# Kernel optimization log

Hardware: AMD Instinct MI355X
Metric: run time of the kernel (lower is better)

## Reference

```python
import jax, jax.numpy as jnp
import numpy as np

E, B, N, F, F1D, H, L, H2, PE_DIM = 4, 16384, 1024, 64, 64, 256, 2, 256, 63
TOPK_MEM = 16      # self.top_K: memory retrieval top-k
W0_SIREN = 30.0    # SIREN omega_0 for 'sine' nonlinearity
NUM_FREQ = 10      # PosEncoding num_frequencies
LINE_DIM = 64      # feat_shapes[0]


def _ln(h, g, b):
    m = jnp.mean(h, axis=-1, keepdims=True)
    v = jnp.mean((h - m) ** 2, axis=-1, keepdims=True)
    return (h - m) / jnp.sqrt(v + 1e-5) * g + b


def _pos_enc(coords):
    # NeRF positional encoding: [coords, sin/cos interleaved per coord per freq]
    freqs = 2.0 ** jnp.arange(NUM_FREQ, dtype=coords.dtype)
    scaled = coords[..., None] * freqs * jnp.pi            # (B, 3, NF)
    sc = jnp.stack([jnp.sin(scaled), jnp.cos(scaled)], axis=-1)  # (B, 3, NF, 2)
    return jnp.concatenate([coords, sc.reshape(coords.shape[0], -1)], axis=-1)  # (B, 63)


def _forward(x, lines, mem_k, mem_v, enc_w0, enc_b0, enc_wh, enc_bh, enc_wo, enc_bo,
             ln_g, ln_b, wq, wk, wv, ad_w0, ad_b0, ad_w1, ad_b1, ad_ln_g, ad_ln_b,
             mg_w0, mg_b0, mg_w1, mg_b1, fw0, fb0, fw1, fb1, fw2, fb2, fw3, fb3, route_k):
    coords = x[:, :3]
    # --- 1D line feature interpolation (param_feats) ---
    p = x[:, 3] * (LINE_DIM - 1)
    pf = jnp.floor(p)
    w = p - pf
    il = pf.astype(jnp.int32)
    ih = jnp.clip(pf + 1.0, 0.0, LINE_DIM - 1).astype(jnp.int32)
    f1d = lines[0][:, il] + w * (lines[0][:, ih] - lines[0][:, il])  # (F1D, B)
    param_feats = f1d.T                                              # (B, F1D)

    pe_x = _pos_enc(coords)                                          # (B, 63)
    scale = float(F) ** 0.5

    def expert(ew0, eb0, ewh, ebh, ewo, ebo, wq_e, wk_e, wv_e, mk, mv,
               aw0, ab0, aw1, ab1, ag, ab):
        # SIREN encoder MLP
        h = jnp.sin(W0_SIREN * (pe_x @ ew0 + eb0))
        for l in range(L):
            h = jnp.sin(W0_SIREN * (h @ ewh[l] + ebh[l]))
        mlp_feats = h @ ewo + ebo                          # (B, F)
        q = _ln(mlp_feats, ln_g, ln_b) @ wq_e              # (B, F)
        kp = mk @ wk_e                                     # (N, F) precomputed keys
        vp = mv @ wv_e                                     # (N, F) precomputed values
        scores = q @ kp.T                                  # (B, N)
        _, idx = jax.lax.top_k(scores, TOPK_MEM)           # (B, K)
        k_top = kp[idx]                                    # (B, K, F)
        v_top = vp[idx]                                    # (B, K, F)
        pfe = jnp.broadcast_to(param_feats[:, None, :], (param_feats.shape[0], TOPK_MEM, F1D))
        a = jnp.concatenate([v_top, pfe], axis=-1)         # (B, K, F+F1D)
        a = jax.nn.relu(a @ aw0 + ab0) @ aw1 + ab1
        adapted = v_top + _ln(a, ag, ab)
        attn = jax.nn.softmax(jnp.einsum('bf,bkf->bk', q, k_top) / scale, axis=-1)
        return jnp.einsum('bk,bkf->bf', attn, adapted) + mlp_feats

    # compute every expert densely (vectorized), then gather routed top-k outputs
    all_out = jax.vmap(expert)(enc_w0, enc_b0, enc_wh, enc_bh, enc_wo, enc_bo,
                               wq, wk, wv, mem_k, mem_v,
                               ad_w0, ad_b0, ad_w1, ad_b1, ad_ln_g, ad_ln_b)  # (E, B, F)

    raw_q = jax.nn.relu(coords @ mg_w0 + mg_b0) @ mg_w1 + mg_b1   # manager_net (B, E)
    probs = jnp.clip(jax.nn.softmax(raw_q, axis=-1), 1e-8, None)
    vals, tidx = jax.lax.top_k(probs, route_k)                    # (B, k)
    vals = vals / jnp.sum(vals, axis=-1, keepdims=True)
    gathered = jnp.take_along_axis(jnp.swapaxes(all_out, 0, 1), tidx[..., None], axis=1)  # (B, k, F)
    spatial = jnp.sum(vals[..., None] * gathered, axis=1)         # (B, F)

    h = jax.nn.relu(spatial @ fw0 + fb0)
    h = jax.nn.relu(h @ fw1 + fb1)
    h = jax.nn.relu(h @ fw2 + fb2)
    refined = jax.nn.sigmoid(h @ fw3 + fb3)
    return refined, raw_q


def setup_inputs() -> dict:
    ks = jax.random.split(jax.random.key(0), 24)
    f32 = jnp.float32
    rn = lambda i, shp, s: jax.random.normal(ks[i], shp, f32) * s
    xav = lambda fi, fo: (2.0 / (fi + fo)) ** 0.5
    return {
        'x': jax.random.uniform(ks[0], (B, 4), f32),
        'lines': jax.random.uniform(ks[1], (1, F1D, LINE_DIM), f32, 0.7, 0.8),
        'mem_k': rn(2, (E, N, F), 1.0),
        'mem_v': rn(3, (E, N, F), 1e-3),
        'enc_w0': rn(4, (E, PE_DIM, H), xav(PE_DIM, H)),
        'enc_b0': jnp.zeros((E, H), f32),
        'enc_wh': rn(5, (E, L, H, H), xav(H, H)),
        'enc_bh': jnp.zeros((E, L, H), f32),
        'enc_wo': rn(6, (E, H, F), xav(H, F)),
        'enc_bo': jnp.zeros((E, F), f32),
        'ln_g': jnp.ones((F,), f32),
        'ln_b': jnp.zeros((F,), f32),
        'wq': rn(7, (E, F, F), xav(F, F)),
        'wk': rn(8, (E, F, F), xav(F, F)),
        'wv': rn(9, (E, F, F), xav(F, F)),
        'ad_w0': rn(10, (E, F + F1D, 64), xav(F + F1D, 64)),
        'ad_b0': rn(11, (E, 64), 1e-3),
        'ad_w1': rn(12, (E, 64, F), xav(64, F)),
        'ad_b1': rn(13, (E, F), 1e-3),
        'ad_ln_g': jnp.ones((E, F), f32),
        'ad_ln_b': jnp.zeros((E, F), f32),
        'mg_w0': rn(14, (3, 64), 0.5),
        'mg_b0': jnp.zeros((64,), f32),
        'mg_w1': rn(15, (64, E), 0.5),
        'mg_b1': jnp.zeros((E,), f32),
        'fw0': rn(16, (F, H2), xav(F, H2)),
        'fb0': rn(17, (H2,), 1e-3),
        'fw1': rn(18, (H2, H2), xav(H2, H2)),
        'fb1': rn(19, (H2,), 1e-3),
        'fw2': rn(20, (H2, H2), xav(H2, H2)),
        'fb2': rn(21, (H2,), 1e-3),
        'fw3': rn(22, (H2, 1), xav(H2, 1)),
        'fb3': rn(23, (1,), 1e-3),
        'route_k': 2,
    }


def reference(x, lines, mem_k, mem_v, enc_w0, enc_b0, enc_wh, enc_bh, enc_wo, enc_bo,
              ln_g, ln_b, wq, wk, wv, ad_w0, ad_b0, ad_w1, ad_b1, ad_ln_g, ad_ln_b,
              mg_w0, mg_b0, mg_w1, mg_b1, fw0, fb0, fw1, fb1, fw2, fb2, fw3, fb3, route_k):
    return _forward(x, lines, mem_k, mem_v, enc_w0, enc_b0, enc_wh, enc_bh, enc_wo, enc_bo,
                    ln_g, ln_b, wq, wk, wv, ad_w0, ad_b0, ad_w1, ad_b1, ad_ln_g, ad_ln_b,
                    mg_w0, mg_b0, mg_w1, mg_b1, fw0, fb0, fw1, fb1, fw2, fb2, fw3, fb3, route_k)
```

## Files before the change

### kernel.cpp

```cpp
#include <hip/hip_runtime.h>
#include <math.h>

#define EE 4
#define BB 16384
#define NN 1024
#define FF 64
#define HH 256
#define PED 63
#define TOPK 16
#define LINE 64
#define TS 32
#define NBX (BB/TS)

#define OFF_KP   0u
#define OFF_VP   262144u
#define OFF_VPA  524288u
#define OFF_PE   786432u
#define OFF_PF   1818624u
#define OFF_EO   2867200u
#define OFF_RW   4964352u
#define OFF_CNT  4997120u
#define OFF_LIST 4997128u
#define OFF_QV   5062664u
#define OFF_SM   7159816u
#define OFF_WP   OFF_EO

__device__ __forceinline__ float wred_sum(float v) {
#pragma unroll
    for (int off = 32; off > 0; off >>= 1) v += __shfl_xor(v, off, 64);
    return v;
}
__device__ __forceinline__ void wred_sum2(float& a, float& b) {
#pragma unroll
    for (int off = 32; off > 0; off >>= 1) {
        a += __shfl_xor(a, off, 64);
        b += __shfl_xor(b, off, 64);
    }
}
__device__ __forceinline__ float rdlane(float v, int k) {
    return __int_as_float(__builtin_amdgcn_readlane(__float_as_int(v), k));
}

__global__ __launch_bounds__(256) void k_prep(
    const float* __restrict__ wv, const float* __restrict__ aw0,
    float* __restrict__ wp)
{
    int e = blockIdx.x;
    __shared__ float sa[FF*FF];
    for (int i = threadIdx.x; i < FF*FF; i += 256)
        sa[i] = aw0[(size_t)e*128*FF + i];
    __syncthreads();
    int f = threadIdx.x & 63, dg = threadIdx.x >> 6;
    for (int d = dg; d < FF; d += 4) {
        const float* wr = wv + (size_t)e*FF*FF + d*FF;
        float a = 0.f;
        for (int c = 0; c < FF; ++c) a = fmaf(wr[c], sa[c*FF+f], a);
        wp[(size_t)e*FF*FF + d*FF + f] = a;
    }
}

__global__ __launch_bounds__(256) void k_proj(
    const float* __restrict__ mem_k, const float* __restrict__ mem_v,
    const float* __restrict__ wk, const float* __restrict__ wv,
    const float* __restrict__ wp,
    float* __restrict__ kp, float* __restrict__ vp, float* __restrict__ vpa)
{
    int e = blockIdx.x >> 6;
    int nbase = (blockIdx.x & 63) * 16;
    __shared__ float swk[FF*FF], swv[FF*FF], swp[FF*FF];
    for (int i = threadIdx.x; i < FF*FF; i += 256) {
        swk[i] = wk[(size_t)e*FF*FF + i];
        swv[i] = wv[(size_t)e*FF*FF + i];
        swp[i] = wp[(size_t)e*FF*FF + i];
    }
    __syncthreads();
    int r4 = threadIdx.x >> 6;
    int f  = threadIdx.x & 63;
#pragma unroll 1
    for (int it = 0; it < 4; ++it) {
        int n = nbase + it*4 + r4;
        const float* mk = mem_k + ((size_t)e*NN + n)*FF;
        const float* mv = mem_v + ((size_t)e*NN + n)*FF;
        float ak = 0.f, av = 0.f, aa = 0.f;
#pragma unroll 1
        for (int c4 = 0; c4 < 16; ++c4) {
            float4 k4 = *(const float4*)&mk[4*c4];
            float4 v4 = *(const float4*)&mv[4*c4];
#pragma unroll
            for (int kk = 0; kk < 4; ++kk) {
                float mkc = (kk==0)?k4.x:((kk==1)?k4.y:((kk==2)?k4.z:k4.w));
                float mvc = (kk==0)?v4.x:((kk==1)?v4.y:((kk==2)?v4.z:v4.w));
                int c = 4*c4 + kk;
                ak = fmaf(mkc, swk[c*FF+f], ak);
                av = fmaf(mvc, swv[c*FF+f], av);
                aa = fmaf(mvc, swp[c*FF+f], aa);
            }
        }
        kp [((size_t)e*NN+n)*FF + f] = ak;
        vp [((size_t)e*NN+n)*FF + f] = av;
        vpa[((size_t)e*NN+n)*FF + f] = aa;
    }
}

__global__ __launch_bounds__(256) void k_route(
    const float* __restrict__ x, const float* __restrict__ lines,
    const float* __restrict__ mg_w0, const float* __restrict__ mg_b0,
    const float* __restrict__ mg_w1, const float* __restrict__ mg_b1,
    float* __restrict__ pe_x, float* __restrict__ pfm,
    float* __restrict__ rawq, float* __restrict__ rw,
    int* __restrict__ counts, int* __restrict__ lists)
{
    __shared__ float slines[LINE*LINE];
    for (int i = threadIdx.x; i < LINE*LINE; i += 256) slines[i] = lines[i];
    __syncthreads();
    int b = blockIdx.x*256 + threadIdx.x;
    float4 xx = ((const float4*)x)[b];
    float c0 = xx.x, c1 = xx.y, c2 = xx.z, c3 = xx.w;

    float p = c3 * (float)(LINE-1);
    float pfl = floorf(p);
    float w = p - pfl;
    int il = (int)pfl;
    int ih = (int)fminf(fmaxf(pfl + 1.f, 0.f), (float)(LINE-1));
    for (int c = 0; c < FF; ++c) {
        float lo = slines[c*LINE+il], hi = slines[c*LINE+ih];
        pfm[(size_t)b*FF + c] = lo + w*(hi-lo);
    }
    float* pe = pe_x + (size_t)b*PED;
    pe[0]=c0; pe[1]=c1; pe[2]=c2;
    const float PI = 3.14159265358979323846f;
    float coords[3] = {c0,c1,c2};
#pragma unroll
    for (int cc = 0; cc < 3; ++cc) {
        float fr = PI;
        for (int k = 0; k < 10; ++k) {
            float s = coords[cc]*fr;
            pe[3 + cc*20 + k*2 + 0] = sinf(s);
            pe[3 + cc*20 + k*2 + 1] = cosf(s);
            fr *= 2.f;
        }
    }
    float acc[4] = {mg_b1[0], mg_b1[1], mg_b1[2], mg_b1[3]};
    for (int j = 0; j < 64; ++j) {
        float h = fmaf(c0, mg_w0[j], fmaf(c1, mg_w0[64+j], fmaf(c2, mg_w0[128+j], mg_b0[j])));
        h = fmaxf(h, 0.f);
#pragma unroll
        for (int e4 = 0; e4 < 4; ++e4) acc[e4] = fmaf(h, mg_w1[j*4+e4], acc[e4]);
    }
#pragma unroll
    for (int e4 = 0; e4 < 4; ++e4) rawq[(size_t)b*4 + e4] = acc[e4];
    float m = fmaxf(fmaxf(acc[0],acc[1]), fmaxf(acc[2],acc[3]));
    float ex[4], den = 0.f;
#pragma unroll
    for (int e4 = 0; e4 < 4; ++e4) { ex[e4] = expf(acc[e4]-m); den += ex[e4]; }
    float pr[4];
#pragma unroll
    for (int e4 = 0; e4 < 4; ++e4) pr[e4] = fmaxf(ex[e4]/den, 1e-8f);
    int i0 = 0;
#pragma unroll
    for (int e4 = 1; e4 < 4; ++e4) if (pr[e4] > pr[i0]) i0 = e4;
    int i1 = -1;
#pragma unroll
    for (int e4 = 0; e4 < 4; ++e4) {
        if (e4 == i0) continue;
        if (i1 < 0 || pr[e4] > pr[i1]) i1 = e4;
    }
    float vs = pr[i0] + pr[i1];
    rw[b*2+0] = pr[i0]/vs;
    rw[b*2+1] = pr[i1]/vs;
    int p0 = atomicAdd(&counts[i0], 1);
    lists[i0*BB + p0] = b*2 + 0;
    int p1 = atomicAdd(&counts[i1], 1);
    lists[i1*BB + p1] = b*2 + 1;
}

__global__ __launch_bounds__(512, 3) void k_mlp(
    const float* __restrict__ pe_x,
    const float* __restrict__ enc_w0, const float* __restrict__ enc_b0,
    const float* __restrict__ enc_wh, const float* __restrict__ enc_bh,
    const float* __restrict__ enc_wo, const float* __restrict__ enc_bo,
    const float* __restrict__ ln_g, const float* __restrict__ ln_b,
    const float* __restrict__ wq,
    const int* __restrict__ counts, const int* __restrict__ lists,
    float* __restrict__ qv, float* __restrict__ smlpw)
{
    const int e = blockIdx.y;
    const int base = blockIdx.x * TS;
    const int cnt = counts[e];
    if (base >= cnt) return;

    __shared__ float sh[TS*HH];
    __shared__ float swt[4096];
    __shared__ int   slist[TS];

    const int tid = threadIdx.x;
    const int lane = tid & 63;
    const int wv = tid >> 6;
    const int r0 = wv*4;

    if (tid < TS) {
        int idx = base + tid;
        if (idx >= cnt) idx = cnt - 1;
        slist[tid] = lists[e*BB + idx];
    }
    __syncthreads();
    for (int i = tid; i < TS*64; i += 512) {
        int s = i >> 6, j = i & 63;
        int bq = slist[s] >> 1;
        sh[s*HH + j] = (j < PED) ? pe_x[(size_t)bq*PED + j] : 0.f;
    }

    float acc[4][4];

    {
        const float* W = enc_w0 + (size_t)e*PED*HH;
#pragma unroll
        for (int s = 0; s < 4; ++s)
#pragma unroll
            for (int j = 0; j < 4; ++j) acc[s][j] = 0.f;
#pragma unroll 1
        for (int t = 0; t < 4; ++t) {
            int rbase = t*16;
            int rows = (PED - rbase < 16) ? (PED - rbase) : 16;
            int total = rows*HH;
            __syncthreads();
            for (int i = tid*4; i < total; i += 2048)
                *(float4*)&swt[i] = *(const float4*)&W[rbase*HH + i];
            __syncthreads();
#pragma unroll 1
            for (int k = 0; k < rows; ++k) {
                float4 w4 = *(const float4*)&swt[k*HH + 4*lane];
#pragma unroll
                for (int s = 0; s < 4; ++s) {
                    float hv = sh[(r0+s)*HH + rbase + k];
                    acc[s][0] = fmaf(hv, w4.x, acc[s][0]);
                    acc[s][1] = fmaf(hv, w4.y, acc[s][1]);
                    acc[s][2] = fmaf(hv, w4.z, acc[s][2]);
                    acc[s][3] = fmaf(hv, w4.w, acc[s][3]);
                }
            }
        }
        __syncthreads();
        float4 b4 = *(const float4*)&enc_b0[e*HH + 4*lane];
#pragma unroll
        for (int s = 0; s < 4; ++s) {
            float4 o;
            o.x = sinf(30.0f*(acc[s][0] + b4.x));
            o.y = sinf(30.0f*(acc[s][1] + b4.y));
            o.z = sinf(30.0f*(acc[s][2] + b4.z));
            o.w = sinf(30.0f*(acc[s][3] + b4.w));
            *(float4*)&sh[(r0+s)*HH + 4*lane] = o;
        }
    }

#pragma unroll 1
    for (int layer = 0; layer < 2; ++layer) {
        const float* W = enc_wh + ((size_t)(e*2+layer))*HH*HH;
#pragma unroll
        for (int s = 0; s < 4; ++s)
#pragma unroll
            for (int j = 0; j < 4; ++j) acc[s][j] = 0.f;
#pragma unroll 1
        for (int t = 0; t < 16; ++t) {
            __syncthreads();
            for (int i = tid*4; i < 4096; i += 2048)
                *(float4*)&swt[i] = *(const float4*)&W[t*16*HH + i];
            __syncthreads();
#pragma unroll 1
            for (int k4 = 0; k4 < 4; ++k4) {
                float4 h4[4];
#pragma unroll
                for (int s = 0; s < 4; ++s)
                    h4[s] = *(const float4*)&sh[(r0+s)*HH + t*16 + 4*k4];
#pragma unroll
                for (int kk = 0; kk < 4; ++kk) {
                    float4 w4 = *(const float4*)&swt[(4*k4+kk)*HH + 4*lane];
#pragma unroll
                    for (int s = 0; s < 4; ++s) {
                        float hv = (kk==0)?h4[s].x:((kk==1)?h4[s].y:((kk==2)?h4[s].z:h4[s].w));
                        acc[s][0] = fmaf(hv, w4.x, acc[s][0]);
                        acc[s][1] = fmaf(hv, w4.y, acc[s][1]);
                        acc[s][2] = fmaf(hv, w4.z, acc[s][2]);
                        acc[s][3] = fmaf(hv, w4.w, acc[s][3]);
                    }
                }
            }
        }
        __syncthreads();
        float4 b4 = *(const float4*)&enc_bh[(e*2+layer)*HH + 4*lane];
#pragma unroll
        for (int s = 0; s < 4; ++s) {
            float4 o;
            o.x = sinf(30.0f*(acc[s][0] + b4.x));
            o.y = sinf(30.0f*(acc[s][1] + b4.y));
            o.z = sinf(30.0f*(acc[s][2] + b4.z));
            o.w = sinf(30.0f*(acc[s][3] + b4.w));
            *(float4*)&sh[(r0+s)*HH + 4*lane] = o;
        }
    }

    float smlp_r[4];
    {
        const float* W = enc_wo + (size_t)e*HH*FF;
        float a2o[4] = {0.f,0.f,0.f,0.f};
#pragma unroll 1
        for (int t = 0; t < 4; ++t) {
            __syncthreads();
            for (int i = tid*4; i < 4096; i += 2048)
                *(float4*)&swt[i] = *(const float4*)&W[t*64*FF + i];
            __syncthreads();
#pragma unroll 1
            for (int k4 = 0; k4 < 16; ++k4) {
                float4 h4[4];
#pragma unroll
                for (int s = 0; s < 4; ++s)
                    h4[s] = *(const float4*)&sh[(r0+s)*HH + t*64 + 4*k4];
#pragma unroll
                for (int kk = 0; kk < 4; ++kk) {
                    float w = swt[(4*k4+kk)*FF + lane];
#pragma unroll
                    for (int s = 0; s < 4; ++s) {
                        float hv = (kk==0)?h4[s].x:((kk==1)?h4[s].y:((kk==2)?h4[s].z:h4[s].w));
                        a2o[s] = fmaf(hv, w, a2o[s]);
                    }
                }
            }
        }
        float bv = enc_bo[e*FF + lane];
#pragma unroll
        for (int s = 0; s < 4; ++s) smlp_r[s] = a2o[s] + bv;
    }

    {
        const float* Wq = wq + (size_t)e*FF*FF;
        __syncthreads();
        for (int i = tid*4; i < 4096; i += 2048)
            *(float4*)&swt[i] = *(const float4*)&Wq[i];
        __syncthreads();
        float g = ln_g[lane], bb2 = ln_b[lane];
#pragma unroll 1
        for (int s = 0; s < 4; ++s) {
            float hv = smlp_r[s];
            float sm = hv, s2 = hv*hv;
            wred_sum2(sm, s2);
            float mean = sm * (1.f/64.f);
            float var = s2 * (1.f/64.f) - mean*mean;
            float lnv = (hv - mean) * rsqrtf(var + 1e-5f) * g + bb2;
            sh[(r0+s)*HH + lane] = lnv;
            float qa = 0.f;
#pragma unroll 1
            for (int c4 = 0; c4 < 16; ++c4) {
                float4 l4 = *(const float4*)&sh[(r0+s)*HH + 4*c4];
                qa = fmaf(l4.x, swt[(4*c4+0)*FF + lane], qa);
                qa = fmaf(l4.y, swt[(4*c4+1)*FF + lane], qa);
                qa = fmaf(l4.z, swt[(4*c4+2)*FF + lane], qa);
                qa = fmaf(l4.w, swt[(4*c4+3)*FF + lane], qa);
            }
            if (base + r0 + s < cnt) {
                size_t entry = (size_t)slist[r0+s];
                qv[entry*FF + lane] = qa;
                smlpw[entry*FF + lane] = smlp_r[s];
            }
        }
    }
}

__global__ __launch_bounds__(512) void k_attn(
    const float* __restrict__ pfm,
    const float* __restrict__ kp, const float* __restrict__ vp,
    const float* __restrict__ vpa,
    const float* __restrict__ qv, const float* __restrict__ smlpw,
    const float* __restrict__ aw0, const float* __restrict__ ab0,
    const float* __restrict__ aw1, const float* __restrict__ ab1,
    const float* __restrict__ adg, const float* __restrict__ adb,
    const int* __restrict__ counts, const int* __restrict__ lists,
    float* __restrict__ eo)
{
    const int e = blockIdx.y;
    const int base = blockIdx.x * TS;
    const int cnt = counts[e];
    if (base >= cnt) return;

    __shared__ float su[8192];
    __shared__ float sa0[4096];
    __shared__ float sw1[4096];
    __shared__ int   slist[TS];

    const int tid = threadIdx.x;
    const int lane = tid & 63;
    const int wv = tid >> 6;
    const int r0 = wv*4;

    if (tid < TS) {
        int idx = base + tid;
        if (idx >= cnt) idx = cnt - 1;
        slist[tid] = lists[e*BB + idx];
    }
    __syncthreads();

    float qf[4];
#pragma unroll
    for (int s = 0; s < 4; ++s)
        qf[s] = qv[(size_t)slist[r0+s]*FF + lane];

    {
        const float* a0bG = aw0 + ((size_t)e*128 + 64)*FF;
        const float* w1G  = aw1 + (size_t)e*FF*FF;
        for (int i = tid*4; i < 4096; i += 2048) {
            *(float4*)&sa0[i] = *(const float4*)&a0bG[i];
            *(float4*)&sw1[i] = *(const float4*)&w1G[i];
        }
    }

    float sc[4][16];
    float* skp = su;
    {
        const float* kpe = kp + (size_t)e*NN*FF;
        const int str = tid >> 3;
        const int stc = (tid & 7) * 8;
        float4 pre0, pre1;
        pre0 = *(const float4*)&kpe[(size_t)(0*64 + str)*FF + stc];
        pre1 = *(const float4*)&kpe[(size_t)(0*64 + str)*FF + stc + 4];
        *(float4*)&skp[str*68 + stc]     = pre0;
        *(float4*)&skp[str*68 + stc + 4] = pre1;
        __syncthreads();
#pragma unroll 1
        for (int c = 0; c < 16; ++c) {
            if (c < 15) {
                pre0 = *(const float4*)&kpe[(size_t)((c+1)*64 + str)*FF + stc];
                pre1 = *(const float4*)&kpe[(size_t)((c+1)*64 + str)*FF + stc + 4];
            }
            float a0 = 0.f, a1 = 0.f, a2s = 0.f, a3 = 0.f;
#pragma unroll
            for (int f4 = 0; f4 < 16; ++f4) {
                float4 k4 = *(const float4*)&skp[lane*68 + 4*f4];
#pragma unroll
                for (int kk = 0; kk < 4; ++kk) {
                    int k = 4*f4 + kk;
                    float kv = (kk==0)?k4.x:((kk==1)?k4.y:((kk==2)?k4.z:k4.w));
                    a0 = fmaf(rdlane(qf[0], k), kv, a0);
                    a1 = fmaf(rdlane(qf[1], k), kv, a1);
                    a2s= fmaf(rdlane(qf[2], k), kv, a2s);
                    a3 = fmaf(rdlane(qf[3], k), kv, a3);
                }
            }
            sc[0][c]=a0; sc[1][c]=a1; sc[2][c]=a2s; sc[3][c]=a3;
            __syncthreads();
            if (c < 15) {
                *(float4*)&skp[str*68 + stc]     = pre0;
                *(float4*)&skp[str*68 + stc + 4] = pre1;
                __syncthreads();
            }
        }
    }
    __syncthreads();

    const float* vpe  = vp  + (size_t)e*NN*FF;
    const float* vpae = vpa + (size_t)e*NN*FF;
    const float agv = adg[e*FF + lane], abv = adb[e*FF + lane];
    const float ab0v = ab0[e*FF + lane];
    const float ab1v = ab1[e*FF + lane];
    float* plw = &su[wv*1024];

#pragma unroll
    for (int u = 0; u < 4; ++u) {
        int s = r0 + u;
        int entry = slist[s];
        int bq = entry >> 1;

        float pp = ab0v;
        {
            const float* pfr = pfm + (size_t)bq*FF;
#pragma unroll 1
            for (int c4 = 0; c4 < 16; ++c4) {
                float4 p4 = *(const float4*)&pfr[4*c4];
                pp = fmaf(p4.x, sa0[(4*c4+0)*FF + lane], pp);
                pp = fmaf(p4.y, sa0[(4*c4+1)*FF + lane], pp);
                pp = fmaf(p4.z, sa0[(4*c4+2)*FF + lane], pp);
                pp = fmaf(p4.w, sa0[(4*c4+3)*FF + lane], pp);
            }
        }

        float wr_my = 0.f; int rn_my = 0;
        unsigned taken = 0u;
        bool need = true;
        float bv = -1e30f; int bn = 0x7fffffff;
        float v0max = 0.f, wsum = 0.f;
#pragma unroll
        for (int r = 0; r < TOPK; ++r) {
            if (need) {
                bv = -1e30f; bn = 0x7fffffff;
#pragma unroll
                for (int c = 0; c < 16; ++c) {
                    float v = sc[u][c];
                    int n = c*64 + lane;
                    bool ok = !((taken >> c) & 1u);
                    bool better = ok && (v > bv || (v == bv && n < bn));
                    bv = better ? v : bv;
                    bn = better ? n : bn;
                }
                need = false;
            }
            float rv = bv; int rn = bn;
#pragma unroll
            for (int off = 32; off > 0; off >>= 1) {
                float ov = __shfl_xor(rv, off, 64);
                int on = __shfl_xor(rn, off, 64);
                bool better = (ov > rv) || (ov == rv && on < rn);
                rv = better ? ov : rv;
                rn = better ? on : rn;
            }
            if (r == 0) v0max = rv;
            float wr = expf((rv - v0max) * 0.125f);
            wsum += wr;
            if ((rn & 63) == lane) { taken |= 1u << (rn >> 6); need = true; }
            if (lane == r) { wr_my = wr; rn_my = rn; }
        }

        float oaccv = 0.f;
#pragma unroll
        for (int b4i = 0; b4i < 4; ++b4i) {
            float pav4[4];
#pragma unroll
            for (int j = 0; j < 4; ++j) {
                int r = b4i*4 + j;
                int rn_b = __shfl(rn_my, r, 64);
                float wr_b = __shfl(wr_my, r, 64);
                pav4[j] = vpae[(size_t)rn_b*FF + lane];
                float vv = vpe[(size_t)rn_b*FF + lane];
                oaccv = fmaf(wr_b, vv, oaccv);
            }
            int slot = b4i ^ (lane & 3);
            float4 o;
            o.x = fmaxf(pav4[0] + pp, 0.f);
            o.y = fmaxf(pav4[1] + pp, 0.f);
            o.z = fmaxf(pav4[2] + pp, 0.f);
            o.w = fmaxf(pav4[3] + pp, 0.f);
            *(float4*)&plw[lane*16 + slot*4] = o;
        }
        float a2[16];
#pragma unroll
        for (int r = 0; r < 16; ++r) a2[r] = ab1v;
#pragma unroll 1
        for (int j4 = 0; j4 < 16; ++j4) {
            const float* plj = &plw[j4*64];
#pragma unroll
            for (int jj = 0; jj < 4; ++jj) {
                float w = sw1[(4*j4+jj)*FF + lane];
#pragma unroll
                for (int lq = 0; lq < 4; ++lq) {
                    float4 d = *(const float4*)&plj[jj*16 + ((lq ^ jj) * 4)];
                    a2[4*lq+0] = fmaf(d.x, w, a2[4*lq+0]);
                    a2[4*lq+1] = fmaf(d.y, w, a2[4*lq+1]);
                    a2[4*lq+2] = fmaf(d.z, w, a2[4*lq+2]);
                    a2[4*lq+3] = fmaf(d.w, w, a2[4*lq+3]);
                }
            }
        }
        float oln = 0.f;
#pragma unroll
        for (int r = 0; r < TOPK; ++r) {
            float av = a2[r];
            float sm = av, s2 = av*av;
            wred_sum2(sm, s2);
            float mean = sm * (1.f/64.f);
            float var = s2 * (1.f/64.f) - mean*mean;
            float lnv = (av - mean) * rsqrtf(var + 1e-5f) * agv + abv;
            float wr_b = __shfl(wr_my, r, 64);
            oln = fmaf(wr_b, lnv, oln);
        }
        float res = (oaccv + oln) / wsum + smlpw[(size_t)entry*FF + lane];
        if (base + s < cnt) eo[(size_t)entry*FF + lane] = res;
    }
}

__global__ __launch_bounds__(512, 3) void k_final(
    const float* __restrict__ eo, const float* __restrict__ rw,
    const float* __restrict__ fw0, const float* __restrict__ fb0,
    const float* __restrict__ fw1, const float* __restrict__ fb1,
    const float* __restrict__ fw2, const float* __restrict__ fb2,
    const float* __restrict__ fw3, const float* __restrict__ fb3,
    float* __restrict__ refined)
{
    __shared__ float sh[TS*HH];
    __shared__ float swt[4096];
    const int tid = threadIdx.x, lane = tid & 63, wv = tid >> 6;
    const int sbase = blockIdx.x * TS;
    const int r0 = wv*4;
    for (int i = tid; i < TS*64; i += 512) {
        int s = i >> 6, c = i & 63;
        int b = sbase + s;
        sh[s*HH + c] = rw[b*2]*eo[(size_t)(b*2)*FF + c]
                     + rw[b*2+1]*eo[(size_t)(b*2+1)*FF + c];
    }
    float acc[4][4];
    {
#pragma unroll
        for (int s = 0; s < 4; ++s)
#pragma unroll
            for (int j = 0; j < 4; ++j) acc[s][j] = 0.f;
#pragma unroll 1
        for (int t = 0; t < 4; ++t) {
            __syncthreads();
            for (int i = tid*4; i < 4096; i += 2048)
                *(float4*)&swt[i] = *(const float4*)&fw0[t*16*HH + i];
            __syncthreads();
#pragma unroll 1
            for (int k = 0; k < 16; ++k) {
                float4 w4 = *(const float4*)&swt[k*HH + 4*lane];
#pragma unroll
                for (int s = 0; s < 4; ++s) {
                    float hv = sh[(r0+s)*HH + t*16 + k];
                    acc[s][0] = fmaf(hv, w4.x, acc[s][0]);
                    acc[s][1] = fmaf(hv, w4.y, acc[s][1]);
                    acc[s][2] = fmaf(hv, w4.z, acc[s][2]);
                    acc[s][3] = fmaf(hv, w4.w, acc[s][3]);
                }
            }
        }
        __syncthreads();
        float4 b4 = *(const float4*)&fb0[4*lane];
#pragma unroll
        for (int s = 0; s < 4; ++s) {
            float4 o;
            o.x = fmaxf(acc[s][0] + b4.x, 0.f);
            o.y = fmaxf(acc[s][1] + b4.y, 0.f);
            o.z = fmaxf(acc[s][2] + b4.z, 0.f);
            o.w = fmaxf(acc[s][3] + b4.w, 0.f);
            *(float4*)&sh[(r0+s)*HH + 4*lane] = o;
        }
    }
#pragma unroll 1
    for (int layer = 0; layer < 2; ++layer) {
        const float* W  = layer ? fw2 : fw1;
        const float* bi = layer ? fb2 : fb1;
#pragma unroll
        for (int s = 0; s < 4; ++s)
#pragma unroll
            for (int j = 0; j < 4; ++j) acc[s][j] = 0.f;
#pragma unroll 1
        for (int t = 0; t < 16; ++t) {
            __syncthreads();
            for (int i = tid*4; i < 4096; i += 2048)
                *(float4*)&swt[i] = *(const float4*)&W[t*16*HH + i];
            __syncthreads();
#pragma unroll 1
            for (int k4 = 0; k4 < 4; ++k4) {
                float4 h4[4];
#pragma unroll
                for (int s = 0; s < 4; ++s)
                    h4[s] = *(const float4*)&sh[(r0+s)*HH + t*16 + 4*k4];
#pragma unroll
                for (int kk = 0; kk < 4; ++kk) {
                    float4 w4 = *(const float4*)&swt[(4*k4+kk)*HH + 4*lane];
#pragma unroll
                    for (int s = 0; s < 4; ++s) {
                        float hv = (kk==0)?h4[s].x:((kk==1)?h4[s].y:((kk==2)?h4[s].z:h4[s].w));
                        acc[s][0] = fmaf(hv, w4.x, acc[s][0]);
                        acc[s][1] = fmaf(hv, w4.y, acc[s][1]);
                        acc[s][2] = fmaf(hv, w4.z, acc[s][2]);
                        acc[s][3] = fmaf(hv, w4.w, acc[s][3]);
                    }
                }
            }
        }
        __syncthreads();
        float4 b4 = *(const float4*)&bi[4*lane];
#pragma unroll
        for (int s = 0; s < 4; ++s) {
            float4 o;
            o.x = fmaxf(acc[s][0] + b4.x, 0.f);
            o.y = fmaxf(acc[s][1] + b4.y, 0.f);
            o.z = fmaxf(acc[s][2] + b4.z, 0.f);
            o.w = fmaxf(acc[s][3] + b4.w, 0.f);
            *(float4*)&sh[(r0+s)*HH + 4*lane] = o;
        }
    }
    {
        float4 w4 = *(const float4*)&fw3[4*lane];
#pragma unroll 1
        for (int s = 0; s < 4; ++s) {
            float4 h4 = *(const float4*)&sh[(r0+s)*HH + 4*lane];
            float part = h4.x*w4.x + h4.y*w4.y + h4.z*w4.z + h4.w*w4.w;
            float tot = wred_sum(part) + fb3[0];
            float r = 1.f/(1.f + expf(-tot));
            if (lane == 0) refined[sbase + r0 + s] = r;
        }
    }
}

extern "C" void kernel_launch(void* const* d_in, const int* in_sizes, int n_in,
                              void* d_out, int out_size, void* d_ws, size_t ws_size,
                              hipStream_t stream)
{
    const float* x      = (const float*)d_in[0];
    const float* lines  = (const float*)d_in[1];
    const float* mem_k  = (const float*)d_in[2];
    const float* mem_v  = (const float*)d_in[3];
    const float* enc_w0 = (const float*)d_in[4];
    const float* enc_b0 = (const float*)d_in[5];
    const float* enc_wh = (const float*)d_in[6];
    const float* enc_bh = (const float*)d_in[7];
    const float* enc_wo = (const float*)d_in[8];
    const float* enc_bo = (const float*)d_in[9];
    const float* ln_g   = (const float*)d_in[10];
    const float* ln_b   = (const float*)d_in[11];
    const float* wq     = (const float*)d_in[12];
    const float* wk     = (const float*)d_in[13];
    const float* wv_    = (const float*)d_in[14];
    const float* ad_w0  = (const float*)d_in[15];
    const float* ad_b0  = (const float*)d_in[16];
    const float* ad_w1  = (const float*)d_in[17];
    const float* ad_b1  = (const float*)d_in[18];
    const float* ad_g   = (const float*)d_in[19];
    const float* ad_b   = (const float*)d_in[20];
    const float* mg_w0  = (const float*)d_in[21];
    const float* mg_b0  = (const float*)d_in[22];
    const float* mg_w1  = (const float*)d_in[23];
    const float* mg_b1  = (const float*)d_in[24];
    const float* fw0    = (const float*)d_in[25];
    const float* fb0    = (const float*)d_in[26];
    const float* fw1    = (const float*)d_in[27];
    const float* fb1    = (const float*)d_in[28];
    const float* fw2    = (const float*)d_in[29];
    const float* fb2    = (const float*)d_in[30];
    const float* fw3    = (const float*)d_in[31];
    const float* fb3    = (const float*)d_in[32];

    float* out_ref = (float*)d_out;
    float* out_rq  = (float*)d_out + BB;

    float* ws  = (float*)d_ws;
    float* kp  = ws + OFF_KP;
    float* vp  = ws + OFF_VP;
    float* vpa = ws + OFF_VPA;
    float* pe  = ws + OFF_PE;
    float* pfm = ws + OFF_PF;
    float* eo  = ws + OFF_EO;
    float* rw  = ws + OFF_RW;
    float* qvw = ws + OFF_QV;
    float* smw = ws + OFF_SM;
    float* wpw = ws + OFF_WP;
    int*  cnts = (int*)(ws + OFF_CNT);
    int*  lst  = (int*)(ws + OFF_LIST);

    hipMemsetAsync(cnts, 0, EE*sizeof(int), stream);
    k_prep<<<dim3(EE), dim3(256), 0, stream>>>(wv_, ad_w0, wpw);
    k_proj<<<dim3(EE*64), dim3(256), 0, stream>>>(mem_k, mem_v, wk, wv_, wpw, kp, vp, vpa);
    k_route<<<dim3(BB/256), dim3(256), 0, stream>>>(x, lines, mg_w0, mg_b0, mg_w1, mg_b1,
                                                    pe, pfm, out_rq, rw, cnts, lst);
    k_mlp<<<dim3(NBX, EE), dim3(512), 0, stream>>>(pe,
        enc_w0, enc_b0, enc_wh, enc_bh, enc_wo, enc_bo, ln_g, ln_b, wq,
        cnts, lst, qvw, smw);
    k_attn<<<dim3(NBX, EE), dim3(512), 0, stream>>>(pfm, kp, vp, vpa, qvw, smw,
        ad_w0, ad_b0, ad_w1, ad_b1, ad_g, ad_b, cnts, lst, eo);
    k_final<<<dim3(BB/TS), dim3(512), 0, stream>>>(eo, rw, fw0, fb0, fw1, fb1,
                                                   fw2, fb2, fw3, fb3, out_ref);
}
```

Baseline: 1.472 ms.

## Store projected keys feature-blocked and stream scores directly from global memory

The key projection now writes keys in a transposed layout, grouped four features at a time, so each lane can read a float4 of four features for one memory row straight from global memory. The score loop no longer stages key tiles in shared memory and no longer needs the block-wide barriers around that staging. Top-k selection for all four rows now runs before the value-gather phase, and the value gathers are batched in groups of eight so more loads are in flight at once. The trade is more global/L2 traffic per block in exchange for fewer barriers, plus extra registers for the hoisted top-k state, which could lower occupancy.

```diff
diff --git a/kernel.cpp b/kernel.cpp
--- a/kernel.cpp
+++ b/kernel.cpp
@@ -63,7 +63,7 @@
     const float* __restrict__ mem_k, const float* __restrict__ mem_v,
     const float* __restrict__ wk, const float* __restrict__ wv,
     const float* __restrict__ wp,
-    float* __restrict__ kp, float* __restrict__ vp, float* __restrict__ vpa)
+    float* __restrict__ kpT4, float* __restrict__ vp, float* __restrict__ vpa)
 {
     int e = blockIdx.x >> 6;
     int nbase = (blockIdx.x & 63) * 16;
@@ -96,7 +96,7 @@
                 aa = fmaf(mvc, swp[c*FF+f], aa);
             }
         }
-        kp [((size_t)e*NN+n)*FF + f] = ak;
+        kpT4[(size_t)e*NN*FF + (size_t)(f>>2)*(NN*4) + (size_t)n*4 + (f&3)] = ak;
         vp [((size_t)e*NN+n)*FF + f] = av;
         vpa[((size_t)e*NN+n)*FF + f] = aa;
     }
@@ -367,7 +367,7 @@
 
 __global__ __launch_bounds__(512) void k_attn(
     const float* __restrict__ pfm,
-    const float* __restrict__ kp, const float* __restrict__ vp,
+    const float* __restrict__ kpT4, const float* __restrict__ vp,
     const float* __restrict__ vpa,
     const float* __restrict__ qv, const float* __restrict__ smlpw,
     const float* __restrict__ aw0, const float* __restrict__ ab0,
@@ -413,75 +413,41 @@
     }
 
     float sc[4][16];
-    float* skp = su;
+#pragma unroll
+    for (int s = 0; s < 4; ++s)
+#pragma unroll
+        for (int c = 0; c < 16; ++c) sc[s][c] = 0.f;
     {
-        const float* kpe = kp + (size_t)e*NN*FF;
-        const int str = tid >> 3;
-        const int stc = (tid & 7) * 8;
-        float4 pre0, pre1;
-        pre0 = *(const float4*)&kpe[(size_t)(0*64 + str)*FF + stc];
-        pre1 = *(const float4*)&kpe[(size_t)(0*64 + str)*FF + stc + 4];
-        *(float4*)&skp[str*68 + stc]     = pre0;
-        *(float4*)&skp[str*68 + stc + 4] = pre1;
-        __syncthreads();
-#pragma unroll 1
-        for (int c = 0; c < 16; ++c) {
-            if (c < 15) {
-                pre0 = *(const float4*)&kpe[(size_t)((c+1)*64 + str)*FF + stc];
-                pre1 = *(const float4*)&kpe[(size_t)((c+1)*64 + str)*FF + stc + 4];
-            }
-            float a0 = 0.f, a1 = 0.f, a2s = 0.f, a3 = 0.f;
-#pragma unroll
-            for (int f4 = 0; f4 < 16; ++f4) {
-                float4 k4 = *(const float4*)&skp[lane*68 + 4*f4];
-#pragma unroll
-                for (int kk = 0; kk < 4; ++kk) {
-                    int k = 4*f4 + kk;
-                    float kv = (kk==0)?k4.x:((kk==1)?k4.y:((kk==2)?k4.z:k4.w));
-                    a0 = fmaf(rdlane(qf[0], k), kv, a0);
-                    a1 = fmaf(rdlane(qf[1], k), kv, a1);
-                    a2s= fmaf(rdlane(qf[2], k), kv, a2s);
-                    a3 = fmaf(rdlane(qf[3], k), kv, a3);
+        const float* kte = kpT4 + (size_t)e*NN*FF;
+#pragma unroll 1
+        for (int f4 = 0; f4 < 16; ++f4) {
+            float qb0[4], qb1[4], qb2[4], qb3[4];
+#pragma unroll
+            for (int s = 0; s < 4; ++s) {
+                qb0[s] = rdlane(qf[s], 4*f4+0);
+                qb1[s] = rdlane(qf[s], 4*f4+1);
+                qb2[s] = rdlane(qf[s], 4*f4+2);
+                qb3[s] = rdlane(qf[s], 4*f4+3);
+            }
+            const float* kf = kte + (size_t)f4*(NN*4);
+#pragma unroll
+            for (int c = 0; c < 16; ++c) {
+                float4 k4 = *(const float4*)&kf[(c*64 + lane)*4];
+#pragma unroll
+                for (int s = 0; s < 4; ++s) {
+                    sc[s][c] = fmaf(qb3[s], k4.w,
+                               fmaf(qb2[s], k4.z,
+                               fmaf(qb1[s], k4.y,
+                               fmaf(qb0[s], k4.x, sc[s][c]))));
                 }
             }
-            sc[0][c]=a0; sc[1][c]=a1; sc[2][c]=a2s; sc[3][c]=a3;
-            __syncthreads();
-            if (c < 15) {
-                *(float4*)&skp[str*68 + stc]     = pre0;
-                *(float4*)&skp[str*68 + stc + 4] = pre1;
-                __syncthreads();
-            }
-        }
-    }
-    __syncthreads();
-
-    const float* vpe  = vp  + (size_t)e*NN*FF;
-    const float* vpae = vpa + (size_t)e*NN*FF;
-    const float agv = adg[e*FF + lane], abv = adb[e*FF + lane];
-    const float ab0v = ab0[e*FF + lane];
-    const float ab1v = ab1[e*FF + lane];
-    float* plw = &su[wv*1024];
-
+        }
+    }
+
+    float wr_my[4]; int rn_my[4]; float wsum_u[4];
 #pragma unroll
     for (int u = 0; u < 4; ++u) {
-        int s = r0 + u;
-        int entry = slist[s];
-        int bq = entry >> 1;
-
-        float pp = ab0v;
-        {
-            const float* pfr = pfm + (size_t)bq*FF;
-#pragma unroll 1
-            for (int c4 = 0; c4 < 16; ++c4) {
-                float4 p4 = *(const float4*)&pfr[4*c4];
-                pp = fmaf(p4.x, sa0[(4*c4+0)*FF + lane], pp);
-                pp = fmaf(p4.y, sa0[(4*c4+1)*FF + lane], pp);
-                pp = fmaf(p4.z, sa0[(4*c4+2)*FF + lane], pp);
-                pp = fmaf(p4.w, sa0[(4*c4+3)*FF + lane], pp);
-            }
-        }
-
-        float wr_my = 0.f; int rn_my = 0;
+        float wr_m = 0.f; int rn_m = 0;
         unsigned taken = 0u;
         bool need = true;
         float bv = -1e30f; int bn = 0x7fffffff;
@@ -514,29 +480,68 @@
             float wr = expf((rv - v0max) * 0.125f);
             wsum += wr;
             if ((rn & 63) == lane) { taken |= 1u << (rn >> 6); need = true; }
-            if (lane == r) { wr_my = wr; rn_my = rn; }
+            if (lane == r) { wr_m = wr; rn_m = rn; }
+        }
+        wr_my[u] = wr_m; rn_my[u] = rn_m; wsum_u[u] = wsum;
+    }
+
+    __syncthreads();
+
+    const float* vpe  = vp  + (size_t)e*NN*FF;
+    const float* vpae = vpa + (size_t)e*NN*FF;
+    const float agv = adg[e*FF + lane], abv = adb[e*FF + lane];
+    const float ab0v = ab0[e*FF + lane];
+    const float ab1v = ab1[e*FF + lane];
+    float* plw = &su[wv*1024];
+
+#pragma unroll
+    for (int u = 0; u < 4; ++u) {
+        int s = r0 + u;
+        int entry = slist[s];
+        int bq = entry >> 1;
+
+        float pp = ab0v;
+        {
+            const float* pfr = pfm + (size_t)bq*FF;
+#pragma unroll 1
+            for (int c4 = 0; c4 < 16; ++c4) {
+                float4 p4 = *(const float4*)&pfr[4*c4];
+                pp = fmaf(p4.x, sa0[(4*c4+0)*FF + lane], pp);
+                pp = fmaf(p4.y, sa0[(4*c4+1)*FF + lane], pp);
+                pp = fmaf(p4.z, sa0[(4*c4+2)*FF + lane], pp);
+                pp = fmaf(p4.w, sa0[(4*c4+3)*FF + lane], pp);
+            }
         }
 
         float oaccv = 0.f;
 #pragma unroll
-        for (int b4i = 0; b4i < 4; ++b4i) {
-            float pav4[4];
-#pragma unroll
-            for (int j = 0; j < 4; ++j) {
-                int r = b4i*4 + j;
-                int rn_b = __shfl(rn_my, r, 64);
-                float wr_b = __shfl(wr_my, r, 64);
-                pav4[j] = vpae[(size_t)rn_b*FF + lane];
-                float vv = vpe[(size_t)rn_b*FF + lane];
-                oaccv = fmaf(wr_b, vv, oaccv);
-            }
-            int slot = b4i ^ (lane & 3);
-            float4 o;
-            o.x = fmaxf(pav4[0] + pp, 0.f);
-            o.y = fmaxf(pav4[1] + pp, 0.f);
-            o.z = fmaxf(pav4[2] + pp, 0.f);
-            o.w = fmaxf(pav4[3] + pp, 0.f);
-            *(float4*)&plw[lane*16 + slot*4] = o;
+        for (int g2 = 0; g2 < 2; ++g2) {
+            int rnb[8]; float wrb[8];
+#pragma unroll
+            for (int j = 0; j < 8; ++j) {
+                rnb[j] = __shfl(rn_my[u], g2*8 + j, 64);
+                wrb[j] = __shfl(wr_my[u], g2*8 + j, 64);
+            }
+            float pav[8], vv[8];
+#pragma unroll
+            for (int j = 0; j < 8; ++j) {
+                pav[j] = vpae[(size_t)rnb[j]*FF + lane];
+                vv[j]  = vpe [(size_t)rnb[j]*FF + lane];
+            }
+#pragma unroll
+            for (int j = 0; j < 8; ++j)
+                oaccv = fmaf(wrb[j], vv[j], oaccv);
+#pragma unroll
+            for (int q = 0; q < 2; ++q) {
+                int qq = g2*2 + q;
+                int slot = qq ^ (lane & 3);
+                float4 o;
+                o.x = fmaxf(pav[4*q+0] + pp, 0.f);
+                o.y = fmaxf(pav[4*q+1] + pp, 0.f);
+                o.z = fmaxf(pav[4*q+2] + pp, 0.f);
+                o.w = fmaxf(pav[4*q+3] + pp, 0.f);
+                *(float4*)&plw[lane*16 + slot*4] = o;
+            }
         }
         float a2[16];
 #pragma unroll
@@ -566,10 +571,10 @@
             float mean = sm * (1.f/64.f);
             float var = s2 * (1.f/64.f) - mean*mean;
             float lnv = (av - mean) * rsqrtf(var + 1e-5f) * agv + abv;
-            float wr_b = __shfl(wr_my, r, 64);
+            float wr_b = __shfl(wr_my[u], r, 64);
             oln = fmaf(wr_b, lnv, oln);
         }
-        float res = (oaccv + oln) / wsum + smlpw[(size_t)entry*FF + lane];
+        float res = (oaccv + oln) / wsum_u[u] + smlpw[(size_t)entry*FF + lane];
         if (base + s < cnt) eo[(size_t)entry*FF + lane] = res;
     }
 }
@@ -731,7 +736,7 @@
     float* out_rq  = (float*)d_out + BB;
 
     float* ws  = (float*)d_ws;
-    float* kp  = ws + OFF_KP;
+    float* kpT = ws + OFF_KP;
     float* vp  = ws + OFF_VP;
     float* vpa = ws + OFF_VPA;
     float* pe  = ws + OFF_PE;
@@ -746,13 +751,13 @@
 
     hipMemsetAsync(cnts, 0, EE*sizeof(int), stream);
     k_prep<<<dim3(EE), dim3(256), 0, stream>>>(wv_, ad_w0, wpw);
-    k_proj<<<dim3(EE*64), dim3(256), 0, stream>>>(mem_k, mem_v, wk, wv_, wpw, kp, vp, vpa);
+    k_proj<<<dim3(EE*64), dim3(256), 0, stream>>>(mem_k, mem_v, wk, wv_, wpw, kpT, vp, vpa);
     k_route<<<dim3(BB/256), dim3(256), 0, stream>>>(x, lines, mg_w0, mg_b0, mg_w1, mg_b1,
                                                     pe, pfm, out_rq, rw, cnts, lst);
     k_mlp<<<dim3(NBX, EE), dim3(512), 0, stream>>>(pe,
         enc_w0, enc_b0, enc_wh, enc_bh, enc_wo, enc_bo, ln_g, ln_b, wq,
         cnts, lst, qvw, smw);
-    k_attn<<<dim3(NBX, EE), dim3(512), 0, stream>>>(pfm, kp, vp, vpa, qvw, smw,
+    k_attn<<<dim3(NBX, EE), dim3(512), 0, stream>>>(pfm, kpT, vp, vpa, qvw, smw,
         ad_w0, ad_b0, ad_w1, ad_b1, ad_g, ad_b, cnts, lst, eo);
     k_final<<<dim3(BB/TS), dim3(512), 0, stream>>>(eo, rw, fw0, fb0, fw1, fb1,
                                                    fw2, fb2, fw3, fb3, out_ref);
```

Result: faster. 1.437 ms (-2.4%).
